# Kernel optimization log

Hardware: AMD Instinct MI355X
Metric: run time of the kernel (lower is better)

## Reference

```python
import jax, jax.numpy as jnp
import numpy as np

EPS = 1e-5
SLOPE = 0.2


def _conv_bn_lrelu(x, w, b, g, be, m, v):
    # 1x1 conv: (B,C,H,W) x (O,C) -> (B,O,H,W), then BN (inference) + LeakyReLU(0.2)
    y = jnp.einsum('bchw,oc->bohw', x, w) + b[None, :, None, None]
    y = g[None, :, None, None] * (y - m[None, :, None, None]) * jax.lax.rsqrt(v[None, :, None, None] + EPS) + be[None, :, None, None]
    return jnp.where(y >= 0, y, SLOPE * y)


def setup_inputs() -> dict:
    key = jax.random.key(0)
    ks = jax.random.split(key, 20)
    B, C, H, W = 8, 64, 256, 256
    d = {}
    d['x'] = jax.random.normal(ks[0], (B, C, H, W), dtype=jnp.float32)
    d['w1'] = jax.random.normal(ks[1], (1, C), dtype=jnp.float32) * 0.1
    d['b1'] = jax.random.normal(ks[2], (1,), dtype=jnp.float32)
    d['g1'] = jax.random.uniform(ks[3], (1,), dtype=jnp.float32) + 0.5
    d['be1'] = jax.random.normal(ks[4], (1,), dtype=jnp.float32)
    d['m1'] = jax.random.normal(ks[5], (1,), dtype=jnp.float32)
    d['v1'] = jax.random.uniform(ks[6], (1,), dtype=jnp.float32) + 0.5
    d['wA'] = jax.random.normal(ks[7], (C, C), dtype=jnp.float32) * 0.1
    d['bA'] = jax.random.normal(ks[8], (C,), dtype=jnp.float32)
    d['gA'] = jax.random.uniform(ks[9], (C,), dtype=jnp.float32) + 0.5
    d['beA'] = jax.random.normal(ks[10], (C,), dtype=jnp.float32)
    d['mA'] = jax.random.normal(ks[11], (C,), dtype=jnp.float32)
    d['vA'] = jax.random.uniform(ks[12], (C,), dtype=jnp.float32) + 0.5
    d['wO'] = jax.random.normal(ks[13], (C, C), dtype=jnp.float32) * 0.1
    d['bO'] = jax.random.normal(ks[14], (C,), dtype=jnp.float32)
    d['gO'] = jax.random.uniform(ks[15], (C,), dtype=jnp.float32) + 0.5
    d['beO'] = jax.random.normal(ks[16], (C,), dtype=jnp.float32)
    d['mO'] = jax.random.normal(ks[17], (C,), dtype=jnp.float32)
    d['vO'] = jax.random.uniform(ks[18], (C,), dtype=jnp.float32) + 0.5
    return d


def reference(x, w1, b1, g1, be1, m1, v1, wA, bA, gA, beA, mA, vA, wO, bO, gO, beO, mO, vO):
    B, C, H, W = x.shape
    # Branch 1: C->1 conv + BN + LeakyReLU, squeeze channel -> (B,H,W)
    C1 = _conv_bn_lrelu(x, w1, b1, g1, be1, m1, v1)[:, 0]  # (B,H,W)
    C1_t = jnp.swapaxes(C1, 1, 2)                           # (B,W,H)
    S1 = jax.nn.softmax(jnp.matmul(C1, C1_t), axis=-1)      # (B,H,H)
    S2 = jax.nn.softmax(jnp.matmul(C1_t, C1), axis=-1)      # (B,W,W)
    # Branch 2: C->C conv + BN + LeakyReLU
    C2 = _conv_bn_lrelu(x, wA, bA, gA, beA, mA, vA)         # (B,C,H,W)
    # Raw row-major reshapes as in the torch code (mixes channel and spatial dims)
    R1 = C2.reshape(B, H, C * W)
    R2 = C2.reshape(B, W, C * H)
    R3 = jnp.matmul(S1, R1).reshape(B, C, H, W)
    R4 = jnp.matmul(S2, R2).reshape(B, C, H, W)
    C3 = _conv_bn_lrelu(R3 + R4, wO, bO, gO, beO, mO, vO)
    out = C2 + C3
    return (out, S1, S2)
```

## Files before the change

### kernel.cpp

```cpp
#include <hip/hip_runtime.h>


#define EPS 1e-5f

typedef __attribute__((ext_vector_type(8))) short bf16x8;
typedef __attribute__((ext_vector_type(4))) float f32x4;

__device__ __forceinline__ unsigned short f2bf(float f){
  union { float f; unsigned int u; } a; a.f = f;
  return (unsigned short)((a.u + 0x7fffu + ((a.u >> 16) & 1u)) >> 16);
}
__device__ __forceinline__ float lrelu(float y){ return y >= 0.f ? y : 0.2f * y; }
__device__ __forceinline__ bf16x8 cvt8(const float* p){
  float4 a = *(const float4*)p;
  float4 b = *(const float4*)(p + 4);
  bf16x8 r;
  r[0] = (short)f2bf(a.x); r[1] = (short)f2bf(a.y); r[2] = (short)f2bf(a.z); r[3] = (short)f2bf(a.w);
  r[4] = (short)f2bf(b.x); r[5] = (short)f2bf(b.y); r[6] = (short)f2bf(b.z); r[7] = (short)f2bf(b.w);
  return r;
}

__global__ __launch_bounds__(256) void k1_c1(
    const float* __restrict__ x, const float* __restrict__ w1,
    const float* __restrict__ pb1, const float* __restrict__ pg1,
    const float* __restrict__ pbe1, const float* __restrict__ pm1,
    const float* __restrict__ pv1,
    float* __restrict__ C1)
{
  const int blk = blockIdx.x;
  const int b = blk >> 6;
  const int n0 = (blk & 63) << 10;
  const int t = threadIdx.x;
  __shared__ float w1s[64];
  if (t < 64) w1s[t] = w1[t];
  __syncthreads();
  const float* xb = x + ((size_t)b << 22);
  const int n = n0 + (t << 2);
  float4 d = {0.f, 0.f, 0.f, 0.f};
  #pragma unroll 16
  for (int c = 0; c < 64; c++){
    const float4 xv = *(const float4*)(xb + ((size_t)c << 16) + n);
    const float wv = w1s[c];
    d.x = fmaf(xv.x, wv, d.x); d.y = fmaf(xv.y, wv, d.y);
    d.z = fmaf(xv.z, wv, d.z); d.w = fmaf(xv.w, wv, d.w);
  }
  const float s1 = pg1[0] * rsqrtf(pv1[0] + EPS);
  const float t1 = (pb1[0] - pm1[0]) * s1 + pbe1[0];
  float4 o;
  o.x = lrelu(d.x * s1 + t1); o.y = lrelu(d.y * s1 + t1);
  o.z = lrelu(d.z * s1 + t1); o.w = lrelu(d.w * s1 + t1);
  *(float4*)(C1 + (b << 16) + n) = o;
}

__global__ __launch_bounds__(256) void k2_gram(const float* __restrict__ C1, float* __restrict__ P)
{
  const int bx = blockIdx.x;
  const int kh = bx & 3;
  const int tile = (bx >> 2) & 15;
  const int which = (bx >> 6) & 1;
  const int b = bx >> 7;
  const int i0 = (tile >> 2) << 6, j0 = (tile & 3) << 6;
  const float* Cb = C1 + (b << 16);
  __shared__ float Al[32][68];
  __shared__ float Bl[32][68];
  const int t = threadIdx.x;
  const int tx = t & 15, ty = t >> 4;
  float acc[4][4];
  #pragma unroll
  for (int i = 0; i < 4; i++)
    #pragma unroll
    for (int j = 0; j < 4; j++) acc[i][j] = 0.f;

  for (int kc = 0; kc < 2; kc++){
    const int k0 = (kh << 6) + (kc << 5);
    __syncthreads();
    if (which == 0){
      const int i = t & 63, kq = t >> 6;
      const float* pa = Cb + (i0 + i)*256 + k0 + kq*8;
      const float* pb = Cb + (j0 + i)*256 + k0 + kq*8;
      #pragma unroll
      for (int u = 0; u < 8; u++){ Al[kq*8+u][i] = pa[u]; Bl[kq*8+u][i] = pb[u]; }
    } else {
      const int k = t >> 3, i8 = (t & 7) << 3;
      const float* pa = Cb + (k0 + k)*256 + i0 + i8;
      const float* pb = Cb + (k0 + k)*256 + j0 + i8;
      *(float4*)&Al[k][i8]   = *(const float4*)pa;
      *(float4*)&Al[k][i8+4] = *(const float4*)(pa+4);
      *(float4*)&Bl[k][i8]   = *(const float4*)pb;
      *(float4*)&Bl[k][i8+4] = *(const float4*)(pb+4);
    }
    __syncthreads();
    #pragma unroll 4
    for (int k = 0; k < 32; k++){
      float4 a4 = *(const float4*)&Al[k][ty << 2];
      float4 b4 = *(const float4*)&Bl[k][tx << 2];
      float av[4] = {a4.x, a4.y, a4.z, a4.w};
      float bw[4] = {b4.x, b4.y, b4.z, b4.w};
      #pragma unroll
      for (int ii = 0; ii < 4; ii++)
        #pragma unroll
        for (int jj = 0; jj < 4; jj++)
          acc[ii][jj] = fmaf(av[ii], bw[jj], acc[ii][jj]);
    }
  }
  float* Go = P + ((size_t)((kh << 4) + which*8 + b) << 16);
  #pragma unroll
  for (int r = 0; r < 4; r++){
    float4 o4 = {acc[r][0], acc[r][1], acc[r][2], acc[r][3]};
    *(float4*)&Go[(i0 + (ty<<2) + r)*256 + j0 + (tx<<2)] = o4;
  }
}

__global__ __launch_bounds__(256) void k2_softmax(const float* __restrict__ P,
    float* __restrict__ S1o, float* __restrict__ S2o,
    unsigned short* __restrict__ Ssum2)
{
  const int bx = blockIdx.x;
  const int b = bx >> 8, i = bx & 255;
  const int j = threadIdx.x;
  float v1 = 0.f, v2 = 0.f;
  #pragma unroll
  for (int kh = 0; kh < 4; kh++){
    v1 += P[((size_t)((kh << 4) + b) << 16) + i*256 + j];
    v2 += P[((size_t)((kh << 4) + 8 + b) << 16) + i*256 + j];
  }
  __shared__ float sm[4], sm2[4], ss[4], ss2[4];
  float a1 = v1, a2 = v2;
  #pragma unroll
  for (int off = 32; off > 0; off >>= 1){
    a1 = fmaxf(a1, __shfl_xor(a1, off));
    a2 = fmaxf(a2, __shfl_xor(a2, off));
  }
  const int wv = j >> 6;
  if ((j & 63) == 0){ sm[wv] = a1; sm2[wv] = a2; }
  __syncthreads();
  const float m1v = fmaxf(fmaxf(sm[0], sm[1]), fmaxf(sm[2], sm[3]));
  const float m2v = fmaxf(fmaxf(sm2[0], sm2[1]), fmaxf(sm2[2], sm2[3]));
  float e1 = __expf(v1 - m1v), e2 = __expf(v2 - m2v);
  float s1 = e1, s2 = e2;
  #pragma unroll
  for (int off = 32; off > 0; off >>= 1){
    s1 += __shfl_xor(s1, off);
    s2 += __shfl_xor(s2, off);
  }
  if ((j & 63) == 0){ ss[wv] = s1; ss2[wv] = s2; }
  __syncthreads();
  const float d1 = ss[0]+ss[1]+ss[2]+ss[3];
  const float d2 = ss2[0]+ss2[1]+ss2[2]+ss2[3];
  const float S1v = e1 / d1, S2v = e2 / d2;
  S1o[((size_t)b << 16) + i*256 + j] = S1v;
  S2o[((size_t)b << 16) + i*256 + j] = S2v;
  const int ip = ((i & 3) << 6) | (i >> 2);
  const int kp = ((j & 3) << 6) | (j >> 2);
  Ssum2[((size_t)b << 16) + ip*256 + kp] = f2bf(S1v + S2v);
}

__global__ __launch_bounds__(256, 3) void k3_main(
    const float* __restrict__ x,
    const float* __restrict__ wA, const float* __restrict__ pbA,
    const float* __restrict__ pgA, const float* __restrict__ pbeA,
    const float* __restrict__ pmA, const float* __restrict__ pvA,
    const unsigned short* __restrict__ Ssum2,
    const float* __restrict__ wO, const float* __restrict__ pbO,
    const float* __restrict__ pgO, const float* __restrict__ pbeO,
    const float* __restrict__ pmO, const float* __restrict__ pvO,
    float* __restrict__ out)
{
  __shared__ unsigned short XL[128][72];
  __shared__ float sAl[64], tAl[64], sOl[64], tOl[64];
  const int blk = blockIdx.x;
  const int b  = blk >> 9;
  const int j0 = (blk & 511) << 5;
  const int t = threadIdx.x;
  const int lane = t & 63, wv = t >> 6;
  const int m = lane & 15, q = lane >> 4;

  if (t < 64){
    const float sA = pgA[t] * rsqrtf(pvA[t] + EPS);
    sAl[t] = sA; tAl[t] = (pbA[t] - pmA[t]) * sA + pbeA[t];
    const float sO = pgO[t] * rsqrtf(pvO[t] + EPS);
    sOl[t] = sO; tOl[t] = (pbO[t] - pmO[t]) * sO + pbeO[t];
  }

  {
    const float* xs = x + ((size_t)b << 22) + ((size_t)lane << 16) + (wv << 14) + j0;
    #pragma unroll
    for (int i = 0; i < 8; i++){
      const float4 xv = *(const float4*)(xs + 4*i);
      const int s = 32*wv + 4*i;
      XL[s+0][lane] = f2bf(xv.x);
      XL[s+1][lane] = f2bf(xv.y);
      XL[s+2][lane] = f2bf(xv.z);
      XL[s+3][lane] = f2bf(xv.w);
    }
  }
  __syncthreads();

  float sAv[4], tAv[4];
  #pragma unroll
  for (int ot = 0; ot < 4; ot++){ sAv[ot] = sAl[16*ot + m]; tAv[ot] = tAl[16*ot + m]; }

  bf16x8 wfrA[4][2];
  #pragma unroll
  for (int ot = 0; ot < 4; ot++)
    #pragma unroll
    for (int ks = 0; ks < 2; ks++)
      wfrA[ot][ks] = cvt8(wA + (16*ot + m)*64 + ks*32 + q*8);

  const f32x4 vzero = {0.f, 0.f, 0.f, 0.f};
  f32x4 c2r[2][4];
  #pragma unroll
  for (int i = 0; i < 2; i++)
    #pragma unroll
    for (int j = 0; j < 4; j++) c2r[i][j] = vzero;

  #pragma unroll
  for (int ks = 0; ks < 2; ks++)
    #pragma unroll
    for (int nt = 0; nt < 2; nt++){
      const bf16x8 af = *(const bf16x8*)&XL[32*wv + 16*nt + m][ks*32 + q*8];
      #pragma unroll
      for (int ot = 0; ot < 4; ot++)
        c2r[nt][ot] = __builtin_amdgcn_mfma_f32_16x16x32_bf16(af, wfrA[ot][ks], c2r[nt][ot], 0, 0, 0);
    }

  #pragma unroll
  for (int nt = 0; nt < 2; nt++)
    #pragma unroll
    for (int ot = 0; ot < 4; ot++){
      #pragma unroll
      for (int r = 0; r < 4; r++){
        const float v = lrelu(c2r[nt][ot][r] * sAv[ot] + tAv[ot]);
        c2r[nt][ot][r] = v;
        XL[32*wv + 16*nt + 4*q + r][16*ot + m] = f2bf(v);
      }
    }
  __syncthreads();

  const unsigned short* Sb = Ssum2 + ((size_t)b << 16);
  f32x4 accT[4][2];
  #pragma unroll
  for (int i = 0; i < 4; i++)
    #pragma unroll
    for (int j = 0; j < 2; j++) accT[i][j] = vzero;

  #pragma unroll
  for (int ks = 0; ks < 8; ks++){
    const int kk = ks*32 + q*8;
    const int rk = kk >> 6;
    const int c0 = kk & 63;
    bf16x8 af[4], bv[2];
    #pragma unroll
    for (int it = 0; it < 4; it++)
      af[it] = *(const bf16x8*)(Sb + (64*wv + 16*it + m)*256 + kk);
    #pragma unroll
    for (int jt = 0; jt < 2; jt++)
      bv[jt] = *(const bf16x8*)&XL[(rk << 5) + 16*jt + m][c0];
    #pragma unroll
    for (int it = 0; it < 4; it++)
      #pragma unroll
      for (int jt = 0; jt < 2; jt++)
        accT[it][jt] = __builtin_amdgcn_mfma_f32_16x16x32_bf16(af[it], bv[jt], accT[it][jt], 0, 0, 0);
  }
  __syncthreads();

  #pragma unroll
  for (int it = 0; it < 4; it++)
    #pragma unroll
    for (int jt = 0; jt < 2; jt++){
      uint2 pk;
      pk.x = (unsigned)f2bf(accT[it][jt][0]) | ((unsigned)f2bf(accT[it][jt][1]) << 16);
      pk.y = (unsigned)f2bf(accT[it][jt][2]) | ((unsigned)f2bf(accT[it][jt][3]) << 16);
      *(uint2*)&XL[32*wv + 16*jt + m][16*it + 4*q] = pk;
    }

  bf16x8 wfrO[4][2];
  #pragma unroll
  for (int ct = 0; ct < 4; ct++)
    #pragma unroll
    for (int k2 = 0; k2 < 2; k2++)
      wfrO[ct][k2] = cvt8(wO + (16*ct + m)*64 + k2*32 + q*8);

  f32x4 acc2[2][4];
  #pragma unroll
  for (int i = 0; i < 2; i++)
    #pragma unroll
    for (int j = 0; j < 4; j++) acc2[i][j] = vzero;

  #pragma unroll
  for (int k2 = 0; k2 < 2; k2++)
    #pragma unroll
    for (int stl = 0; stl < 2; stl++){
      const bf16x8 afT = *(const bf16x8*)&XL[32*wv + 16*stl + m][k2*32 + q*8];
      #pragma unroll
      for (int ct = 0; ct < 4; ct++)
        acc2[stl][ct] = __builtin_amdgcn_mfma_f32_16x16x32_bf16(afT, wfrO[ct][k2], acc2[stl][ct], 0, 0, 0);
    }

  float sOv[4], tOv[4];
  #pragma unroll
  for (int ct = 0; ct < 4; ct++){ sOv[ct] = sOl[16*ct + m]; tOv[ct] = tOl[16*ct + m]; }

  const size_t outB = ((size_t)b << 22);
  #pragma unroll
  for (int stl = 0; stl < 2; stl++)
    #pragma unroll
    for (int ct = 0; ct < 4; ct++){
      const int cout = 16*ct + m;
      const int ng0 = (wv << 14) + j0 + 16*stl + 4*q;
      float* po = out + outB + ((size_t)cout << 16) + ng0;
      float4 pk;
      pk.x = c2r[stl][ct][0] + lrelu(acc2[stl][ct][0] * sOv[ct] + tOv[ct]);
      pk.y = c2r[stl][ct][1] + lrelu(acc2[stl][ct][1] * sOv[ct] + tOv[ct]);
      pk.z = c2r[stl][ct][2] + lrelu(acc2[stl][ct][2] * sOv[ct] + tOv[ct]);
      pk.w = c2r[stl][ct][3] + lrelu(acc2[stl][ct][3] * sOv[ct] + tOv[ct]);
      *(float4*)po = pk;
    }
}

extern "C" void kernel_launch(void* const* d_in, const int* in_sizes, int n_in,
                              void* d_out, int out_size, void* d_ws, size_t ws_size,
                              hipStream_t stream) {
  const float* x   = (const float*)d_in[0];
  const float* w1  = (const float*)d_in[1];
  const float* b1  = (const float*)d_in[2];
  const float* g1  = (const float*)d_in[3];
  const float* be1 = (const float*)d_in[4];
  const float* m1  = (const float*)d_in[5];
  const float* v1  = (const float*)d_in[6];
  const float* wA  = (const float*)d_in[7];
  const float* bA  = (const float*)d_in[8];
  const float* gA  = (const float*)d_in[9];
  const float* beA = (const float*)d_in[10];
  const float* mA  = (const float*)d_in[11];
  const float* vA  = (const float*)d_in[12];
  const float* wO  = (const float*)d_in[13];
  const float* bO  = (const float*)d_in[14];
  const float* gO  = (const float*)d_in[15];
  const float* beO = (const float*)d_in[16];
  const float* mO  = (const float*)d_in[17];
  const float* vO  = (const float*)d_in[18];

  float* out = (float*)d_out;

  char* ws = (char*)d_ws;
  float* C1             = (float*)(ws);
  unsigned short* Ssum2 = (unsigned short*)(ws + (size_t)(6u << 20));

  k1_c1<<<dim3(512), dim3(256), 0, stream>>>(x, w1, b1, g1, be1, m1, v1, C1);
  k2_gram<<<dim3(1024), dim3(256), 0, stream>>>(C1, out);
  k2_softmax<<<dim3(2048), dim3(256), 0, stream>>>(out, out + 33554432u, out + 34078720u, Ssum2);
  k3_main<<<dim3(4096), dim3(256), 0, stream>>>(x, wA, bA, gA, beA, mA, vA, Ssum2,
                                                wO, bO, gO, beO, mO, vO, out);
}
```

Before: 416.4 us.

## Double k3 tile width, load x directly into MFMA fragments, split T GEMM

The main kernel now covers 64 spatial columns per block instead of 32, halving the grid, and reuses the Ssum2 row fragments across twice as many columns. The x tile is no longer staged through LDS: each lane gathers scalar x values straight from global memory into bf16 MFMA operands. The S·C2 product is split into two halves to limit live accumulators, and the output conv is done in two passes. The C1 kernel processes two elements per thread with twice as many blocks. The trade-off is uncoalesced scalar global loads for x, higher register pressure and lower occupancy, in exchange for fewer blocks and less redundant Ssum2 traffic.

New measurement: 401.2 us. 3.6% less time.

```diff
diff --git a/kernel.cpp b/kernel.cpp
--- a/kernel.cpp
+++ b/kernel.cpp
@@ -28,28 +28,26 @@
     float* __restrict__ C1)
 {
   const int blk = blockIdx.x;
-  const int b = blk >> 6;
-  const int n0 = (blk & 63) << 10;
+  const int b = blk >> 7;
+  const int n0 = (blk & 127) << 9;
   const int t = threadIdx.x;
   __shared__ float w1s[64];
   if (t < 64) w1s[t] = w1[t];
   __syncthreads();
   const float* xb = x + ((size_t)b << 22);
-  const int n = n0 + (t << 2);
-  float4 d = {0.f, 0.f, 0.f, 0.f};
+  const int n = n0 + (t << 1);
+  float2 d = {0.f, 0.f};
   #pragma unroll 16
   for (int c = 0; c < 64; c++){
-    const float4 xv = *(const float4*)(xb + ((size_t)c << 16) + n);
+    const float2 xv = *(const float2*)(xb + ((size_t)c << 16) + n);
     const float wv = w1s[c];
     d.x = fmaf(xv.x, wv, d.x); d.y = fmaf(xv.y, wv, d.y);
-    d.z = fmaf(xv.z, wv, d.z); d.w = fmaf(xv.w, wv, d.w);
   }
   const float s1 = pg1[0] * rsqrtf(pv1[0] + EPS);
   const float t1 = (pb1[0] - pm1[0]) * s1 + pbe1[0];
-  float4 o;
+  float2 o;
   o.x = lrelu(d.x * s1 + t1); o.y = lrelu(d.y * s1 + t1);
-  o.z = lrelu(d.z * s1 + t1); o.w = lrelu(d.w * s1 + t1);
-  *(float4*)(C1 + (b << 16) + n) = o;
+  *(float2*)(C1 + (b << 16) + n) = o;
 }
 
 __global__ __launch_bounds__(256) void k2_gram(const float* __restrict__ C1, float* __restrict__ P)
@@ -166,11 +164,11 @@
     const float* __restrict__ pmO, const float* __restrict__ pvO,
     float* __restrict__ out)
 {
-  __shared__ unsigned short XL[128][72];
+  __shared__ unsigned short XL[256][72];
   __shared__ float sAl[64], tAl[64], sOl[64], tOl[64];
   const int blk = blockIdx.x;
-  const int b  = blk >> 9;
-  const int j0 = (blk & 511) << 5;
+  const int b  = blk >> 8;
+  const int j0 = (blk & 255) << 6;
   const int t = threadIdx.x;
   const int lane = t & 63, wv = t >> 6;
   const int m = lane & 15, q = lane >> 4;
@@ -181,19 +179,6 @@
     const float sO = pgO[t] * rsqrtf(pvO[t] + EPS);
     sOl[t] = sO; tOl[t] = (pbO[t] - pmO[t]) * sO + pbeO[t];
   }
-
-  {
-    const float* xs = x + ((size_t)b << 22) + ((size_t)lane << 16) + (wv << 14) + j0;
-    #pragma unroll
-    for (int i = 0; i < 8; i++){
-      const float4 xv = *(const float4*)(xs + 4*i);
-      const int s = 32*wv + 4*i;
-      XL[s+0][lane] = f2bf(xv.x);
-      XL[s+1][lane] = f2bf(xv.y);
-      XL[s+2][lane] = f2bf(xv.z);
-      XL[s+3][lane] = f2bf(xv.w);
-    }
-  }
   __syncthreads();
 
   float sAv[4], tAv[4];
@@ -208,70 +193,115 @@
       wfrA[ot][ks] = cvt8(wA + (16*ot + m)*64 + ks*32 + q*8);
 
   const f32x4 vzero = {0.f, 0.f, 0.f, 0.f};
-  f32x4 c2r[2][4];
-  #pragma unroll
-  for (int i = 0; i < 2; i++)
+  f32x4 c2r[4][4];
+  #pragma unroll
+  for (int i = 0; i < 4; i++)
     #pragma unroll
     for (int j = 0; j < 4; j++) c2r[i][j] = vzero;
 
+  const float* xb = x + ((size_t)b << 22) + (wv << 14) + j0;
   #pragma unroll
   for (int ks = 0; ks < 2; ks++)
     #pragma unroll
-    for (int nt = 0; nt < 2; nt++){
-      const bf16x8 af = *(const bf16x8*)&XL[32*wv + 16*nt + m][ks*32 + q*8];
+    for (int nt = 0; nt < 4; nt++){
+      bf16x8 af;
+      #pragma unroll
+      for (int u = 0; u < 8; u++){
+        const int c = ks*32 + q*8 + u;
+        af[u] = (short)f2bf(xb[((size_t)c << 16) + 16*nt + m]);
+      }
       #pragma unroll
       for (int ot = 0; ot < 4; ot++)
         c2r[nt][ot] = __builtin_amdgcn_mfma_f32_16x16x32_bf16(af, wfrA[ot][ks], c2r[nt][ot], 0, 0, 0);
     }
 
   #pragma unroll
-  for (int nt = 0; nt < 2; nt++)
+  for (int nt = 0; nt < 4; nt++)
     #pragma unroll
     for (int ot = 0; ot < 4; ot++){
       #pragma unroll
       for (int r = 0; r < 4; r++){
         const float v = lrelu(c2r[nt][ot][r] * sAv[ot] + tAv[ot]);
         c2r[nt][ot][r] = v;
-        XL[32*wv + 16*nt + 4*q + r][16*ot + m] = f2bf(v);
+        XL[64*wv + 16*nt + 4*q + r][16*ot + m] = f2bf(v);
       }
     }
   __syncthreads();
 
   const unsigned short* Sb = Ssum2 + ((size_t)b << 16);
-  f32x4 accT[4][2];
-  #pragma unroll
-  for (int i = 0; i < 4; i++)
-    #pragma unroll
-    for (int j = 0; j < 2; j++) accT[i][j] = vzero;
-
+
+  uint2 tp0[2][4];
+  {
+    f32x4 aT[2][4];
+    #pragma unroll
+    for (int i = 0; i < 2; i++)
+      #pragma unroll
+      for (int j = 0; j < 4; j++) aT[i][j] = vzero;
+    #pragma unroll
+    for (int ks = 0; ks < 8; ks++){
+      const int kk = ks*32 + q*8;
+      const int rk = kk >> 6;
+      const int c0 = kk & 63;
+      bf16x8 af2[2], bv[4];
+      #pragma unroll
+      for (int i = 0; i < 2; i++)
+        af2[i] = *(const bf16x8*)(Sb + (64*wv + 16*i + m)*256 + kk);
+      #pragma unroll
+      for (int jt = 0; jt < 4; jt++)
+        bv[jt] = *(const bf16x8*)&XL[(rk << 6) + 16*jt + m][c0];
+      #pragma unroll
+      for (int i = 0; i < 2; i++)
+        #pragma unroll
+        for (int jt = 0; jt < 4; jt++)
+          aT[i][jt] = __builtin_amdgcn_mfma_f32_16x16x32_bf16(af2[i], bv[jt], aT[i][jt], 0, 0, 0);
+    }
+    #pragma unroll
+    for (int i = 0; i < 2; i++)
+      #pragma unroll
+      for (int jt = 0; jt < 4; jt++){
+        tp0[i][jt].x = (unsigned)f2bf(aT[i][jt][0]) | ((unsigned)f2bf(aT[i][jt][1]) << 16);
+        tp0[i][jt].y = (unsigned)f2bf(aT[i][jt][2]) | ((unsigned)f2bf(aT[i][jt][3]) << 16);
+      }
+  }
+
+  f32x4 aTb[2][4];
+  #pragma unroll
+  for (int i = 0; i < 2; i++)
+    #pragma unroll
+    for (int j = 0; j < 4; j++) aTb[i][j] = vzero;
   #pragma unroll
   for (int ks = 0; ks < 8; ks++){
     const int kk = ks*32 + q*8;
     const int rk = kk >> 6;
     const int c0 = kk & 63;
-    bf16x8 af[4], bv[2];
-    #pragma unroll
-    for (int it = 0; it < 4; it++)
-      af[it] = *(const bf16x8*)(Sb + (64*wv + 16*it + m)*256 + kk);
-    #pragma unroll
-    for (int jt = 0; jt < 2; jt++)
-      bv[jt] = *(const bf16x8*)&XL[(rk << 5) + 16*jt + m][c0];
-    #pragma unroll
-    for (int it = 0; it < 4; it++)
-      #pragma unroll
-      for (int jt = 0; jt < 2; jt++)
-        accT[it][jt] = __builtin_amdgcn_mfma_f32_16x16x32_bf16(af[it], bv[jt], accT[it][jt], 0, 0, 0);
-  }
-  __syncthreads();
-
-  #pragma unroll
-  for (int it = 0; it < 4; it++)
-    #pragma unroll
-    for (int jt = 0; jt < 2; jt++){
+    bf16x8 af2[2], bv[4];
+    #pragma unroll
+    for (int i = 0; i < 2; i++)
+      af2[i] = *(const bf16x8*)(Sb + (64*wv + 16*(2 + i) + m)*256 + kk);
+    #pragma unroll
+    for (int jt = 0; jt < 4; jt++)
+      bv[jt] = *(const bf16x8*)&XL[(rk << 6) + 16*jt + m][c0];
+    #pragma unroll
+    for (int i = 0; i < 2; i++)
+      #pragma unroll
+      for (int jt = 0; jt < 4; jt++)
+        aTb[i][jt] = __builtin_amdgcn_mfma_f32_16x16x32_bf16(af2[i], bv[jt], aTb[i][jt], 0, 0, 0);
+  }
+  __syncthreads();
+
+  #pragma unroll
+  for (int i = 0; i < 2; i++)
+    #pragma unroll
+    for (int jt = 0; jt < 4; jt++)
+      *(uint2*)&XL[64*wv + 16*jt + m][16*i + 4*q] = tp0[i][jt];
+  #pragma unroll
+  for (int i = 0; i < 2; i++)
+    #pragma unroll
+    for (int jt = 0; jt < 4; jt++){
       uint2 pk;
-      pk.x = (unsigned)f2bf(accT[it][jt][0]) | ((unsigned)f2bf(accT[it][jt][1]) << 16);
-      pk.y = (unsigned)f2bf(accT[it][jt][2]) | ((unsigned)f2bf(accT[it][jt][3]) << 16);
-      *(uint2*)&XL[32*wv + 16*jt + m][16*it + 4*q] = pk;
+      pk.x = (unsigned)f2bf(aTb[i][jt][0]) | ((unsigned)f2bf(aTb[i][jt][1]) << 16);
+      pk.y = (unsigned)f2bf(aTb[i][jt][2]) | ((unsigned)f2bf(aTb[i][jt][3]) << 16);
+      *(uint2*)&XL[64*wv + 16*jt + m][16*(2 + i) + 4*q] = pk;
     }
 
   bf16x8 wfrO[4][2];
@@ -281,41 +311,44 @@
     for (int k2 = 0; k2 < 2; k2++)
       wfrO[ct][k2] = cvt8(wO + (16*ct + m)*64 + k2*32 + q*8);
 
-  f32x4 acc2[2][4];
-  #pragma unroll
-  for (int i = 0; i < 2; i++)
-    #pragma unroll
-    for (int j = 0; j < 4; j++) acc2[i][j] = vzero;
-
-  #pragma unroll
-  for (int k2 = 0; k2 < 2; k2++)
-    #pragma unroll
-    for (int stl = 0; stl < 2; stl++){
-      const bf16x8 afT = *(const bf16x8*)&XL[32*wv + 16*stl + m][k2*32 + q*8];
-      #pragma unroll
-      for (int ct = 0; ct < 4; ct++)
-        acc2[stl][ct] = __builtin_amdgcn_mfma_f32_16x16x32_bf16(afT, wfrO[ct][k2], acc2[stl][ct], 0, 0, 0);
-    }
-
   float sOv[4], tOv[4];
   #pragma unroll
   for (int ct = 0; ct < 4; ct++){ sOv[ct] = sOl[16*ct + m]; tOv[ct] = tOl[16*ct + m]; }
 
   const size_t outB = ((size_t)b << 22);
   #pragma unroll
-  for (int stl = 0; stl < 2; stl++)
-    #pragma unroll
-    for (int ct = 0; ct < 4; ct++){
-      const int cout = 16*ct + m;
-      const int ng0 = (wv << 14) + j0 + 16*stl + 4*q;
-      float* po = out + outB + ((size_t)cout << 16) + ng0;
-      float4 pk;
-      pk.x = c2r[stl][ct][0] + lrelu(acc2[stl][ct][0] * sOv[ct] + tOv[ct]);
-      pk.y = c2r[stl][ct][1] + lrelu(acc2[stl][ct][1] * sOv[ct] + tOv[ct]);
-      pk.z = c2r[stl][ct][2] + lrelu(acc2[stl][ct][2] * sOv[ct] + tOv[ct]);
-      pk.w = c2r[stl][ct][3] + lrelu(acc2[stl][ct][3] * sOv[ct] + tOv[ct]);
-      *(float4*)po = pk;
-    }
+  for (int h = 0; h < 2; h++){
+    f32x4 a2[2][4];
+    #pragma unroll
+    for (int i = 0; i < 2; i++)
+      #pragma unroll
+      for (int j = 0; j < 4; j++) a2[i][j] = vzero;
+    #pragma unroll
+    for (int k2 = 0; k2 < 2; k2++)
+      #pragma unroll
+      for (int s2 = 0; s2 < 2; s2++){
+        const int stl = 2*h + s2;
+        const bf16x8 afT = *(const bf16x8*)&XL[64*wv + 16*stl + m][k2*32 + q*8];
+        #pragma unroll
+        for (int ct = 0; ct < 4; ct++)
+          a2[s2][ct] = __builtin_amdgcn_mfma_f32_16x16x32_bf16(afT, wfrO[ct][k2], a2[s2][ct], 0, 0, 0);
+      }
+    #pragma unroll
+    for (int s2 = 0; s2 < 2; s2++)
+      #pragma unroll
+      for (int ct = 0; ct < 4; ct++){
+        const int stl = 2*h + s2;
+        const int cout = 16*ct + m;
+        const int ng0 = (wv << 14) + j0 + 16*stl + 4*q;
+        float* po = out + outB + ((size_t)cout << 16) + ng0;
+        float4 pk;
+        pk.x = c2r[stl][ct][0] + lrelu(a2[s2][ct][0] * sOv[ct] + tOv[ct]);
+        pk.y = c2r[stl][ct][1] + lrelu(a2[s2][ct][1] * sOv[ct] + tOv[ct]);
+        pk.z = c2r[stl][ct][2] + lrelu(a2[s2][ct][2] * sOv[ct] + tOv[ct]);
+        pk.w = c2r[stl][ct][3] + lrelu(a2[s2][ct][3] * sOv[ct] + tOv[ct]);
+        *(float4*)po = pk;
+      }
+  }
 }
 
 extern "C" void kernel_launch(void* const* d_in, const int* in_sizes, int n_in,
@@ -347,9 +380,9 @@
   float* C1             = (float*)(ws);
   unsigned short* Ssum2 = (unsigned short*)(ws + (size_t)(6u << 20));
 
-  k1_c1<<<dim3(512), dim3(256), 0, stream>>>(x, w1, b1, g1, be1, m1, v1, C1);
+  k1_c1<<<dim3(1024), dim3(256), 0, stream>>>(x, w1, b1, g1, be1, m1, v1, C1);
   k2_gram<<<dim3(1024), dim3(256), 0, stream>>>(C1, out);
   k2_softmax<<<dim3(2048), dim3(256), 0, stream>>>(out, out + 33554432u, out + 34078720u, Ssum2);
-  k3_main<<<dim3(4096), dim3(256), 0, stream>>>(x, wA, bA, gA, beA, mA, vA, Ssum2,
+  k3_main<<<dim3(2048), dim3(256), 0, stream>>>(x, wA, bA, gA, beA, mA, vA, Ssum2,
                                                 wO, bO, gO, beO, mO, vO, out);
 }
```
